# Kernel tuning notes

Measured on AMD Instinct MI355X. Metric: run time of the kernel, lower is better.

## Reference

```python
import jax, jax.numpy as jnp
import numpy as np

N_NODES = 100000
N_EDGES = 3200000
D_IN = 256
D_OUT = 256


def setup_inputs() -> dict:
    key = jax.random.key(0)
    k1, k2, k3, k4, k5 = jax.random.split(key, 5)
    X = jax.random.normal(k1, (N_NODES, D_IN), dtype=jnp.float32)
    A_rows = jax.random.randint(k2, (N_EDGES,), 0, N_NODES, dtype=jnp.int64)
    A_cols = jax.random.randint(k3, (N_EDGES,), 0, N_NODES, dtype=jnp.int64)
    A_vals = jax.random.uniform(k4, (N_EDGES,), dtype=jnp.float32)
    # Xavier-uniform init of nn.Linear(in_dim, out_dim, bias=False): W is [out, in]
    limit = float(np.sqrt(6.0 / (D_IN + D_OUT)))
    W = jax.random.uniform(k5, (D_OUT, D_IN), minval=-limit, maxval=limit,
                           dtype=jnp.float32)
    return {"X": X, "A_rows": A_rows, "A_cols": A_cols, "A_vals": A_vals, "W": W}


def reference(X, A_rows, A_cols, A_vals, W):
    # AX = A_coo @ X : gather source features, scale by edge value, scatter-add by row
    msgs = X[A_cols] * A_vals[:, None]                  # [E, D_in]
    AX = jax.ops.segment_sum(msgs, A_rows, num_segments=N_NODES)  # [N, D_in]
    # Linear (bias=False) then ReLU; dropout p=0.0 is identity
    H = jax.nn.relu(AX @ W.T)                           # [N, D_out]
    return H
```

## Files before the change

### kernel.cpp

```cpp
#include <hip/hip_runtime.h>
#include <hip/hip_bf16.h>

#define N_NODES 100000
#define N_EDGES 3200000
#define D 256
#define SHIFT 9
#define NBC 196
#define CAP 18000
#define EPB 4096
#define NSPLIT 782
#define NGEMM 1563

typedef __attribute__((ext_vector_type(8))) short short8;
typedef __attribute__((ext_vector_type(4))) float f32x4;

__device__ inline short bfbits(float x) {
    __hip_bfloat16 h = __float2bfloat16(x);
    return __builtin_bit_cast(short, h);
}

__device__ inline short8 load_cvt8(const float* __restrict__ p) {
    float4 a = *(const float4*)p;
    float4 b = *(const float4*)(p + 4);
    short8 r;
    r[0] = bfbits(a.x); r[1] = bfbits(a.y); r[2] = bfbits(a.z); r[3] = bfbits(a.w);
    r[4] = bfbits(b.x); r[5] = bfbits(b.y); r[6] = bfbits(b.z); r[7] = bfbits(b.w);
    return r;
}

__device__ inline int block_excl_scan_256(int c, int* wsum, int& total) {
    const int lane = threadIdx.x & 63, wid = threadIdx.x >> 6;
    int v = c;
    #pragma unroll
    for (int off = 1; off < 64; off <<= 1) {
        int u = __shfl_up(v, off);
        if (lane >= off) v += u;
    }
    if (lane == 63) wsum[wid] = v;
    __syncthreads();
    int w0 = wsum[0], w1 = wsum[1], w2 = wsum[2], w3 = wsum[3];
    total = w0 + w1 + w2 + w3;
    int wex = (wid > 0 ? w0 : 0) + (wid > 1 ? w1 : 0) + (wid > 2 ? w2 : 0);
    return wex + v - c;
}

__global__ __launch_bounds__(256) void init_cursor(int* __restrict__ gcursor)
{
    int t = threadIdx.x;
    if (t < NBC) gcursor[t] = t * CAP;
}

__global__ __launch_bounds__(256) void bucket_split(
    const int* __restrict__ rows, const int* __restrict__ cols,
    const float* __restrict__ vals, int* __restrict__ gcursor,
    int2* __restrict__ bcv, int nE)
{
    __shared__ int cnt[256];
    __shared__ int startp[256];
    __shared__ int posp[256];
    __shared__ int gb[256];
    __shared__ int wsum[4];
    __shared__ int2 scv[EPB];
    const int t  = threadIdx.x;
    const int e0 = blockIdx.x * EPB;

    cnt[t] = 0;
    __syncthreads();

    int  myb[16];
    int2 mycv[16];
    #pragma unroll
    for (int k = 0; k < 16; ++k) {
        int e = e0 + k * 256 + t;
        if (e < nE) {
            int r = rows[e];
            myb[k]  = r >> SHIFT;
            mycv[k] = make_int2(((r & 511) << 17) | cols[e],
                                __float_as_int(vals[e]));
            atomicAdd(&cnt[myb[k]], 1);
        } else {
            myb[k] = -1;
        }
    }
    __syncthreads();

    int c = cnt[t];
    int total;
    int ex = block_excl_scan_256(c, wsum, total);
    startp[t] = ex;
    posp[t]   = ex;
    if (t < NBC && c) gb[t] = atomicAdd(&gcursor[t], c);
    __syncthreads();

    #pragma unroll
    for (int k = 0; k < 16; ++k) {
        if (myb[k] >= 0) {
            int p = atomicAdd(&posp[myb[k]], 1);
            scv[p] = mycv[k];
        }
    }
    __syncthreads();

    const int lane = t & 63, wid = t >> 6;
    for (int b = wid; b < NBC; b += 4) {
        int cb = cnt[b];
        if (!cb) continue;
        int st = startp[b], g = gb[b];
        int lim = (b + 1) * CAP;
        if (g + cb > lim) cb = lim > g ? lim - g : 0;
        for (int i = lane; i < cb; i += 64)
            bcv[g + i] = scv[st + i];
    }
}

__global__ __launch_bounds__(256) void csr_gemm(
    const int* __restrict__ gcursor, const int2* __restrict__ bcv,
    int* __restrict__ rs, int* __restrict__ re, int2* __restrict__ cedge,
    const float* __restrict__ X, const float* __restrict__ W,
    unsigned short* __restrict__ Y)
{
    if (blockIdx.x < NBC) {
        __shared__ int hist[512];
        __shared__ int cur[512];
        __shared__ int wsum[4];
        const int t = threadIdx.x;
        const int b = blockIdx.x;
        const int s = b * CAP, e = gcursor[b];
        const int r0 = b << SHIFT;

        hist[t] = 0; hist[t + 256] = 0;
        __syncthreads();
        for (int j = s + t; j < e; j += 256)
            atomicAdd(&hist[(unsigned)bcv[j].x >> 17], 1);
        __syncthreads();

        int c0 = hist[2 * t], c1 = hist[2 * t + 1];
        int total;
        int ex = block_excl_scan_256(c0 + c1, wsum, total);
        cur[2 * t]     = s + ex;
        cur[2 * t + 1] = s + ex + c0;
        int r = r0 + 2 * t;
        if (r < N_NODES) {
            rs[r] = s + ex;
            re[r] = s + ex + c0;
        }
        if (r + 1 < N_NODES) {
            rs[r + 1] = s + ex + c0;
            re[r + 1] = s + ex + c0 + c1;
        }
        __syncthreads();

        for (int j = s + t; j < e; j += 256) {
            int2 q = bcv[j];
            int p = atomicAdd(&cur[(unsigned)q.x >> 17], 1);
            cedge[p] = q;
        }
    } else {
        const int bid  = blockIdx.x - NBC;
        const int wid  = threadIdx.x >> 6;
        const int lane = threadIdx.x & 63;
        const int m0   = bid * 64;
        const int n0   = wid * 64;
        const int lr   = lane & 15;
        const int ko   = (lane >> 4) * 8;
        const int M    = N_NODES;

        f32x4 acc[4][4] = {};

        #pragma unroll
        for (int k0 = 0; k0 < 256; k0 += 32) {
            short8 bfrag[4], afrag[4];
            #pragma unroll
            for (int j = 0; j < 4; ++j)
                bfrag[j] = load_cvt8(W + (size_t)(n0 + j * 16 + lr) * 256 + k0 + ko);
            #pragma unroll
            for (int i = 0; i < 4; ++i) {
                int r = m0 + i * 16 + lr;
                if (r > M - 1) r = M - 1;
                afrag[i] = load_cvt8(X + (size_t)r * 256 + k0 + ko);
            }
            #pragma unroll
            for (int i = 0; i < 4; ++i)
                #pragma unroll
                for (int j = 0; j < 4; ++j)
                    acc[i][j] = __builtin_amdgcn_mfma_f32_16x16x32_bf16(
                        afrag[i], bfrag[j], acc[i][j], 0, 0, 0);
        }

        #pragma unroll
        for (int i = 0; i < 4; ++i) {
            int rbase = m0 + i * 16 + (lane >> 4) * 4;
            #pragma unroll
            for (int rr = 0; rr < 4; ++rr) {
                int r = rbase + rr;
                if (r < M) {
                    #pragma unroll
                    for (int j = 0; j < 4; ++j)
                        Y[(size_t)r * 256 + n0 + j * 16 + lr] =
                            (unsigned short)bfbits(acc[i][j][rr]);
                }
            }
        }
    }
}

__global__ __launch_bounds__(256) void spmm_gather_relu(
    const unsigned short* __restrict__ Y,
    const int* __restrict__ rs, const int* __restrict__ re,
    const int2* __restrict__ cedge,
    float* __restrict__ H)
{
    int row  = blockIdx.x * 4 + (threadIdx.x >> 6);
    int lane = threadIdx.x & 63;
    if (row >= N_NODES) return;
    int s = rs[row];
    int e = re[row];

    float4 acc = make_float4(0.f, 0.f, 0.f, 0.f);
    const int fo = lane * 4;

    for (int base = s; base < e; base += 64) {
        int idx = base + lane;
        int2 q = make_int2(0, 0);
        if (idx < e) q = cedge[idx];
        int cnt = min(64, e - base);
        int j = 0;
        for (; j + 4 <= cnt; j += 4) {
            int c0 = __builtin_amdgcn_readfirstlane(__shfl(q.x, j))     & 0x1FFFF;
            int c1 = __builtin_amdgcn_readfirstlane(__shfl(q.x, j + 1)) & 0x1FFFF;
            int c2 = __builtin_amdgcn_readfirstlane(__shfl(q.x, j + 2)) & 0x1FFFF;
            int c3 = __builtin_amdgcn_readfirstlane(__shfl(q.x, j + 3)) & 0x1FFFF;
            float v0 = __int_as_float(__builtin_amdgcn_readfirstlane(__shfl(q.y, j)));
            float v1 = __int_as_float(__builtin_amdgcn_readfirstlane(__shfl(q.y, j + 1)));
            float v2 = __int_as_float(__builtin_amdgcn_readfirstlane(__shfl(q.y, j + 2)));
            float v3 = __int_as_float(__builtin_amdgcn_readfirstlane(__shfl(q.y, j + 3)));
            ushort4 y0 = *(const ushort4*)(Y + (size_t)c0 * 256 + fo);
            ushort4 y1 = *(const ushort4*)(Y + (size_t)c1 * 256 + fo);
            ushort4 y2 = *(const ushort4*)(Y + (size_t)c2 * 256 + fo);
            ushort4 y3 = *(const ushort4*)(Y + (size_t)c3 * 256 + fo);
            acc.x += __uint_as_float((unsigned)y0.x << 16) * v0;
            acc.y += __uint_as_float((unsigned)y0.y << 16) * v0;
            acc.z += __uint_as_float((unsigned)y0.z << 16) * v0;
            acc.w += __uint_as_float((unsigned)y0.w << 16) * v0;
            acc.x += __uint_as_float((unsigned)y1.x << 16) * v1;
            acc.y += __uint_as_float((unsigned)y1.y << 16) * v1;
            acc.z += __uint_as_float((unsigned)y1.z << 16) * v1;
            acc.w += __uint_as_float((unsigned)y1.w << 16) * v1;
            acc.x += __uint_as_float((unsigned)y2.x << 16) * v2;
            acc.y += __uint_as_float((unsigned)y2.y << 16) * v2;
            acc.z += __uint_as_float((unsigned)y2.z << 16) * v2;
            acc.w += __uint_as_float((unsigned)y2.w << 16) * v2;
            acc.x += __uint_as_float((unsigned)y3.x << 16) * v3;
            acc.y += __uint_as_float((unsigned)y3.y << 16) * v3;
            acc.z += __uint_as_float((unsigned)y3.z << 16) * v3;
            acc.w += __uint_as_float((unsigned)y3.w << 16) * v3;
        }
        for (; j < cnt; ++j) {
            int   cj = __builtin_amdgcn_readfirstlane(__shfl(q.x, j)) & 0x1FFFF;
            float vj = __int_as_float(__builtin_amdgcn_readfirstlane(__shfl(q.y, j)));
            ushort4 y4 = *(const ushort4*)(Y + (size_t)cj * 256 + fo);
            acc.x += __uint_as_float((unsigned)y4.x << 16) * vj;
            acc.y += __uint_as_float((unsigned)y4.y << 16) * vj;
            acc.z += __uint_as_float((unsigned)y4.z << 16) * vj;
            acc.w += __uint_as_float((unsigned)y4.w << 16) * vj;
        }
    }
    float4 r;
    r.x = acc.x > 0.f ? acc.x : 0.f;
    r.y = acc.y > 0.f ? acc.y : 0.f;
    r.z = acc.z > 0.f ? acc.z : 0.f;
    r.w = acc.w > 0.f ? acc.w : 0.f;
    ((float4*)(H + (size_t)row * 256))[lane] = r;
}


extern "C" void kernel_launch(void* const* d_in, const int* in_sizes, int n_in,
                              void* d_out, int out_size, void* d_ws, size_t ws_size,
                              hipStream_t stream) {
    const float* X    = (const float*)d_in[0];
    const int*   rows = (const int*)d_in[1];
    const int*   cols = (const int*)d_in[2];
    const float* vals = (const float*)d_in[3];
    const float* W    = (const float*)d_in[4];
    float*       H    = (float*)d_out;

    char* ws = (char*)d_ws;
    unsigned short* Y       = (unsigned short*)(ws);
    int2*           bcv     = (int2*)(ws + 51200000);
    int2*           cedge   = (int2*)(ws + 79424000);
    int*            rs      = (int*)(ws + 107648000);
    int*            re      = (int*)(ws + 108048128);
    int*            gcursor = (int*)(ws + 108448256);

    init_cursor<<<1, 256, 0, stream>>>(gcursor);
    bucket_split<<<NSPLIT, 256, 0, stream>>>(rows, cols, vals, gcursor, bcv, N_EDGES);
    csr_gemm<<<NBC + NGEMM, 256, 0, stream>>>(gcursor, bcv, rs, re, cedge, X, W, Y);
    spmm_gather_relu<<<(N_NODES + 3) / 4, 256, 0, stream>>>(Y, rs, re, cedge, H);
}
```

Before: 411.0 us.

## Replace per-bucket CSR build with fixed-slot per-row edge lists, overlap split with GEMM

Moves the GEMM into the same launch as the bucket split, so the X·W product runs alongside edge bucketing instead of alongside the per-bucket histogram and scan. Replaces the histogram, scan and compaction step with a global-atomic row_scatter that writes each edge into a fixed 80-slot region per row, which the gather kernel then reads. This removes the dependency on the CSR build at the cost of global atomics, a larger strided edge buffer and an extra memset. Rows with more than 80 edges would silently drop edges, which is a correctness risk if the degree distribution has a long tail. A fallback path keeps the old CSR pipeline when the workspace is too small.

```diff
diff --git a/kernel.cpp b/kernel.cpp
--- a/kernel.cpp
+++ b/kernel.cpp
@@ -3,10 +3,10 @@
 
 #define N_NODES 100000
 #define N_EDGES 3200000
-#define D 256
 #define SHIFT 9
 #define NBC 196
 #define CAP 18000
+#define CAP_ROW 80
 #define EPB 4096
 #define NSPLIT 782
 #define NGEMM 1563
@@ -44,13 +44,8 @@
     return wex + v - c;
 }
 
-__global__ __launch_bounds__(256) void init_cursor(int* __restrict__ gcursor)
-{
-    int t = threadIdx.x;
-    if (t < NBC) gcursor[t] = t * CAP;
-}
-
-__global__ __launch_bounds__(256) void bucket_split(
+
+__device__ void do_split(int bid,
     const int* __restrict__ rows, const int* __restrict__ cols,
     const float* __restrict__ vals, int* __restrict__ gcursor,
     int2* __restrict__ bcv, int nE)
@@ -62,7 +57,7 @@
     __shared__ int wsum[4];
     __shared__ int2 scv[EPB];
     const int t  = threadIdx.x;
-    const int e0 = blockIdx.x * EPB;
+    const int e0 = bid * EPB;
 
     cnt[t] = 0;
     __syncthreads();
@@ -113,109 +108,60 @@
     }
 }
 
-__global__ __launch_bounds__(256) void csr_gemm(
-    const int* __restrict__ gcursor, const int2* __restrict__ bcv,
-    int* __restrict__ rs, int* __restrict__ re, int2* __restrict__ cedge,
+__device__ void do_gemm(int bid,
     const float* __restrict__ X, const float* __restrict__ W,
     unsigned short* __restrict__ Y)
 {
-    if (blockIdx.x < NBC) {
-        __shared__ int hist[512];
-        __shared__ int cur[512];
-        __shared__ int wsum[4];
-        const int t = threadIdx.x;
-        const int b = blockIdx.x;
-        const int s = b * CAP, e = gcursor[b];
-        const int r0 = b << SHIFT;
-
-        hist[t] = 0; hist[t + 256] = 0;
-        __syncthreads();
-        for (int j = s + t; j < e; j += 256)
-            atomicAdd(&hist[(unsigned)bcv[j].x >> 17], 1);
-        __syncthreads();
-
-        int c0 = hist[2 * t], c1 = hist[2 * t + 1];
-        int total;
-        int ex = block_excl_scan_256(c0 + c1, wsum, total);
-        cur[2 * t]     = s + ex;
-        cur[2 * t + 1] = s + ex + c0;
-        int r = r0 + 2 * t;
-        if (r < N_NODES) {
-            rs[r] = s + ex;
-            re[r] = s + ex + c0;
-        }
-        if (r + 1 < N_NODES) {
-            rs[r + 1] = s + ex + c0;
-            re[r + 1] = s + ex + c0 + c1;
-        }
-        __syncthreads();
-
-        for (int j = s + t; j < e; j += 256) {
-            int2 q = bcv[j];
-            int p = atomicAdd(&cur[(unsigned)q.x >> 17], 1);
-            cedge[p] = q;
-        }
-    } else {
-        const int bid  = blockIdx.x - NBC;
-        const int wid  = threadIdx.x >> 6;
-        const int lane = threadIdx.x & 63;
-        const int m0   = bid * 64;
-        const int n0   = wid * 64;
-        const int lr   = lane & 15;
-        const int ko   = (lane >> 4) * 8;
-        const int M    = N_NODES;
-
-        f32x4 acc[4][4] = {};
-
+    const int wid  = threadIdx.x >> 6;
+    const int lane = threadIdx.x & 63;
+    const int m0   = bid * 64;
+    const int n0   = wid * 64;
+    const int lr   = lane & 15;
+    const int ko   = (lane >> 4) * 8;
+    const int M    = N_NODES;
+
+    f32x4 acc[4][4] = {};
+
+    #pragma unroll
+    for (int k0 = 0; k0 < 256; k0 += 32) {
+        short8 bfrag[4], afrag[4];
         #pragma unroll
-        for (int k0 = 0; k0 < 256; k0 += 32) {
-            short8 bfrag[4], afrag[4];
+        for (int j = 0; j < 4; ++j)
+            bfrag[j] = load_cvt8(W + (size_t)(n0 + j * 16 + lr) * 256 + k0 + ko);
+        #pragma unroll
+        for (int i = 0; i < 4; ++i) {
+            int r = m0 + i * 16 + lr;
+            if (r > M - 1) r = M - 1;
+            afrag[i] = load_cvt8(X + (size_t)r * 256 + k0 + ko);
+        }
+        #pragma unroll
+        for (int i = 0; i < 4; ++i)
             #pragma unroll
             for (int j = 0; j < 4; ++j)
-                bfrag[j] = load_cvt8(W + (size_t)(n0 + j * 16 + lr) * 256 + k0 + ko);
-            #pragma unroll
-            for (int i = 0; i < 4; ++i) {
-                int r = m0 + i * 16 + lr;
-                if (r > M - 1) r = M - 1;
-                afrag[i] = load_cvt8(X + (size_t)r * 256 + k0 + ko);
-            }
-            #pragma unroll
-            for (int i = 0; i < 4; ++i)
+                acc[i][j] = __builtin_amdgcn_mfma_f32_16x16x32_bf16(
+                    afrag[i], bfrag[j], acc[i][j], 0, 0, 0);
+    }
+
+    #pragma unroll
+    for (int i = 0; i < 4; ++i) {
+        int rbase = m0 + i * 16 + (lane >> 4) * 4;
+        #pragma unroll
+        for (int rr = 0; rr < 4; ++rr) {
+            int r = rbase + rr;
+            if (r < M) {
                 #pragma unroll
                 for (int j = 0; j < 4; ++j)
-                    acc[i][j] = __builtin_amdgcn_mfma_f32_16x16x32_bf16(
-                        afrag[i], bfrag[j], acc[i][j], 0, 0, 0);
-        }
-
-        #pragma unroll
-        for (int i = 0; i < 4; ++i) {
-            int rbase = m0 + i * 16 + (lane >> 4) * 4;
-            #pragma unroll
-            for (int rr = 0; rr < 4; ++rr) {
-                int r = rbase + rr;
-                if (r < M) {
-                    #pragma unroll
-                    for (int j = 0; j < 4; ++j)
-                        Y[(size_t)r * 256 + n0 + j * 16 + lr] =
-                            (unsigned short)bfbits(acc[i][j][rr]);
-                }
+                    Y[(size_t)r * 256 + n0 + j * 16 + lr] =
+                        (unsigned short)bfbits(acc[i][j][rr]);
             }
         }
     }
 }
 
-__global__ __launch_bounds__(256) void spmm_gather_relu(
-    const unsigned short* __restrict__ Y,
-    const int* __restrict__ rs, const int* __restrict__ re,
-    const int2* __restrict__ cedge,
-    float* __restrict__ H)
-{
-    int row  = blockIdx.x * 4 + (threadIdx.x >> 6);
-    int lane = threadIdx.x & 63;
-    if (row >= N_NODES) return;
-    int s = rs[row];
-    int e = re[row];
-
+__device__ void gather_core(
+    const unsigned short* __restrict__ Y, const int2* __restrict__ cedge,
+    float* __restrict__ H, int row, int s, int e, int lane)
+{
     float4 acc = make_float4(0.f, 0.f, 0.f, 0.f);
     const int fo = lane * 4;
 
@@ -274,6 +220,122 @@
 }
 
 
+__global__ __launch_bounds__(256) void init_cursor(int* __restrict__ gcursor)
+{
+    int t = threadIdx.x;
+    if (t < NBC) gcursor[t] = t * CAP;
+}
+
+
+__global__ __launch_bounds__(256) void split_gemm(
+    const int* __restrict__ rows, const int* __restrict__ cols,
+    const float* __restrict__ vals, int* __restrict__ gcursor,
+    int2* __restrict__ bcv,
+    const float* __restrict__ X, const float* __restrict__ W,
+    unsigned short* __restrict__ Y, int nE)
+{
+    if (blockIdx.x < NSPLIT)
+        do_split(blockIdx.x, rows, cols, vals, gcursor, bcv, nE);
+    else
+        do_gemm(blockIdx.x - NSPLIT, X, W, Y);
+}
+
+__global__ __launch_bounds__(256) void row_scatter(
+    const int* __restrict__ gcursor, const int2* __restrict__ bcv,
+    int* __restrict__ rowcur, int2* __restrict__ cedge)
+{
+    const int b  = blockIdx.x >> 3;
+    const int s8 = blockIdx.x & 7;
+    const int s  = b * CAP;
+    int e = gcursor[b];
+    int lim = s + CAP;
+    if (e > lim) e = lim;
+    for (int j = s + s8 * 256 + threadIdx.x; j < e; j += 8 * 256) {
+        int2 q = bcv[j];
+        int r = (b << SHIFT) | ((unsigned)q.x >> 17);
+        int p = atomicAdd(&rowcur[r], 1);
+        if (p < CAP_ROW)
+            cedge[(size_t)r * CAP_ROW + p] = q;
+    }
+}
+
+__global__ __launch_bounds__(256) void spmm_gather_slot(
+    const unsigned short* __restrict__ Y,
+    const int* __restrict__ rowcur, const int2* __restrict__ cedge,
+    float* __restrict__ H)
+{
+    int row  = blockIdx.x * 4 + (threadIdx.x >> 6);
+    int lane = threadIdx.x & 63;
+    if (row >= N_NODES) return;
+    int s = row * CAP_ROW;
+    int deg = rowcur[row];
+    if (deg > CAP_ROW) deg = CAP_ROW;
+    gather_core(Y, cedge, H, row, s, s + deg, lane);
+}
+
+
+__global__ __launch_bounds__(256) void bucket_split(
+    const int* __restrict__ rows, const int* __restrict__ cols,
+    const float* __restrict__ vals, int* __restrict__ gcursor,
+    int2* __restrict__ bcv, int nE)
+{
+    do_split(blockIdx.x, rows, cols, vals, gcursor, bcv, nE);
+}
+
+__global__ __launch_bounds__(256) void csr_gemm(
+    const int* __restrict__ gcursor, const int2* __restrict__ bcv,
+    int* __restrict__ rs, int* __restrict__ re, int2* __restrict__ cedge,
+    const float* __restrict__ X, const float* __restrict__ W,
+    unsigned short* __restrict__ Y)
+{
+    if (blockIdx.x < NBC) {
+        __shared__ int hist[512];
+        __shared__ int cur[512];
+        __shared__ int wsum[4];
+        const int t = threadIdx.x;
+        const int b = blockIdx.x;
+        const int s = b * CAP, e = gcursor[b];
+        const int r0 = b << SHIFT;
+
+        hist[t] = 0; hist[t + 256] = 0;
+        __syncthreads();
+        for (int j = s + t; j < e; j += 256)
+            atomicAdd(&hist[(unsigned)bcv[j].x >> 17], 1);
+        __syncthreads();
+
+        int c0 = hist[2 * t], c1 = hist[2 * t + 1];
+        int total;
+        int ex = block_excl_scan_256(c0 + c1, wsum, total);
+        cur[2 * t]     = s + ex;
+        cur[2 * t + 1] = s + ex + c0;
+        int r = r0 + 2 * t;
+        if (r < N_NODES)     { rs[r]     = s + ex;      re[r]     = s + ex + c0; }
+        if (r + 1 < N_NODES) { rs[r + 1] = s + ex + c0; re[r + 1] = s + ex + c0 + c1; }
+        __syncthreads();
+
+        for (int j = s + t; j < e; j += 256) {
+            int2 q = bcv[j];
+            int p = atomicAdd(&cur[(unsigned)q.x >> 17], 1);
+            cedge[p] = q;
+        }
+    } else {
+        do_gemm(blockIdx.x - NBC, X, W, Y);
+    }
+}
+
+__global__ __launch_bounds__(256) void spmm_gather_rsre(
+    const unsigned short* __restrict__ Y,
+    const int* __restrict__ rs, const int* __restrict__ re,
+    const int2* __restrict__ cedge,
+    float* __restrict__ H)
+{
+    int row  = blockIdx.x * 4 + (threadIdx.x >> 6);
+    int lane = threadIdx.x & 63;
+    if (row >= N_NODES) return;
+    gather_core(Y, cedge, H, row, rs[row], re[row], lane);
+}
+
+
 extern "C" void kernel_launch(void* const* d_in, const int* in_sizes, int n_in,
                               void* d_out, int out_size, void* d_ws, size_t ws_size,
                               hipStream_t stream) {
@@ -283,17 +345,33 @@
     const float* vals = (const float*)d_in[3];
     const float* W    = (const float*)d_in[4];
     float*       H    = (float*)d_out;
-
-    char* ws = (char*)d_ws;
-    unsigned short* Y       = (unsigned short*)(ws);
-    int2*           bcv     = (int2*)(ws + 51200000);
-    int2*           cedge   = (int2*)(ws + 79424000);
-    int*            rs      = (int*)(ws + 107648000);
-    int*            re      = (int*)(ws + 108048128);
-    int*            gcursor = (int*)(ws + 108448256);
-
-    init_cursor<<<1, 256, 0, stream>>>(gcursor);
-    bucket_split<<<NSPLIT, 256, 0, stream>>>(rows, cols, vals, gcursor, bcv, N_EDGES);
-    csr_gemm<<<NBC + NGEMM, 256, 0, stream>>>(gcursor, bcv, rs, re, cedge, X, W, Y);
-    spmm_gather_relu<<<(N_NODES + 3) / 4, 256, 0, stream>>>(Y, rs, re, cedge, H);
-}
+    char*        ws   = (char*)d_ws;
+
+    const size_t NEEDED = 143825152;
+
+    unsigned short* Y   = (unsigned short*)(ws);
+    int2*           bcv = (int2*)(ws + 51200000);
+
+    if (ws_size >= NEEDED) {
+        int2* cedge   = (int2*)(ws + 79424000);
+        int*  rowcur  = (int*)(ws + 143424000);
+        int*  gcursor = (int*)(ws + 143824128);
+
+        hipMemsetAsync(rowcur, 0, (size_t)N_NODES * sizeof(int), stream);
+        init_cursor<<<1, 256, 0, stream>>>(gcursor);
+        split_gemm<<<NSPLIT + NGEMM, 256, 0, stream>>>(
+            rows, cols, vals, gcursor, bcv, X, W, Y, N_EDGES);
+        row_scatter<<<NBC * 8, 256, 0, stream>>>(gcursor, bcv, rowcur, cedge);
+        spmm_gather_slot<<<(N_NODES + 3) / 4, 256, 0, stream>>>(Y, rowcur, cedge, H);
+    } else {
+        int2* cedge   = (int2*)(ws + 79424000);
+        int*  rs      = (int*)(ws + 107648000);
+        int*  re      = (int*)(ws + 108048128);
+        int*  gcursor = (int*)(ws + 108448256);
+
+        init_cursor<<<1, 256, 0, stream>>>(gcursor);
+        bucket_split<<<NSPLIT, 256, 0, stream>>>(rows, cols, vals, gcursor, bcv, N_EDGES);
+        csr_gemm<<<NBC + NGEMM, 256, 0, stream>>>(gcursor, bcv, rs, re, cedge, X, W, Y);
+        spmm_gather_rsre<<<(N_NODES + 3) / 4, 256, 0, stream>>>(Y, rs, re, cedge, H);
+    }
+}
```

New measurement: 640.3 us. +55.8%, slower.
